# Performance work log

Measured on AMD Instinct MI355X. Metric: run time of the kernel, lower is better.

## Reference

```python
import jax, jax.numpy as jnp
import numpy as np

B, T, D = 16, 4096, 256


def setup_inputs() -> dict:
    key = jax.random.key(0)
    ks = jax.random.split(key, 10)
    s = 1.0 / np.sqrt(D)  # torch nn.Linear default init range
    inp = {
        "x": jax.random.normal(ks[0], (B, T, D), jnp.float32),
        "hidden": jax.random.normal(ks[1], (B, D), jnp.float32),
    }
    names = ["W0", "b0", "W1", "b1", "W2", "b2", "W3", "b3"]
    for i, n in enumerate(names):
        shape = (D, D) if n.startswith("W") else (D,)
        inp[n] = jax.random.uniform(ks[2 + i], shape, jnp.float32, -s, s)
    return inp


def _gln(x, W0, b0, W1, b1, W2, b2, W3, b3):
    # Two gated-linear blocks; the final Linear(hyper[-1], hidden_size) in the
    # original module is never applied by calc_gln (index == len-1 is skipped).
    h = (x @ W0.T + b0) * jax.nn.sigmoid(x @ W1.T + b1)
    return (h @ W2.T + b2) * jax.nn.sigmoid(h @ W3.T + b3)


def reference(x, hidden, W0, b0, W1, b1, W2, b2, W3, b3):
    b = _gln(x, W0, b0, W1, b1, W2, b2, W3, b3)  # [B, T, D]
    bt = jnp.swapaxes(b, 0, 1)  # [T, B, D] for time-major scan
    init = jax.nn.relu(bt[0] + jnp.roll(hidden, 1, -1))

    def step(prev, b_t):
        out = jax.nn.relu(b_t + jnp.roll(prev, 1, -1))
        return out, out

    last, ys = jax.lax.scan(step, init, bt[1:])
    outputs = jnp.concatenate([init[None], ys], axis=0)  # [T, B, D]
    outputs = jnp.swapaxes(outputs, 0, 1)  # [B, T, D]; squeeze(2) is a no-op for D>1
    return outputs, last
```

## Files before the change

kernel.cpp:

```cpp
#include <hip/hip_runtime.h>
#include <hip/hip_bf16.h>
#include <cstdint>
#include <cstddef>

typedef __bf16 bf16x8 __attribute__((ext_vector_type(8)));
typedef float  f32x4  __attribute__((ext_vector_type(4)));

static constexpr int B  = 16;
static constexpr int T  = 4096;
static constexpr int D  = 256;
static constexpr int M  = B * T;
static constexpr int SEGS = 64;
static constexpr int SEGL = T / SEGS;

__global__ void cvt_w(const float* __restrict__ W0, const float* __restrict__ W1,
                      const float* __restrict__ W2, const float* __restrict__ W3,
                      __bf16* __restrict__ wp) {
    int i = blockIdx.x * blockDim.x + threadIdx.x;
    int s    = i >> 14;
    int r    = i & 16383;
    int ks   = r >> 11;
    int fg   = (r >> 6) & 31;
    int lane = r & 63;
    int kg = lane >> 4, rl = lane & 15;
    int w = fg >> 2, f = fg & 3;
    int q = f >> 1, gate = f & 1;
    int rc = w * 32 + 2 * rl + q;
    const float* src = (s == 0) ? (gate ? W1 : W0) : (gate ? W3 : W2);
    const float* p = src + (size_t)rc * 256 + ks * 32 + kg * 8;
    bf16x8 o;
#pragma unroll
    for (int j = 0; j < 8; ++j) o[j] = (__bf16)p[j];
    *reinterpret_cast<bf16x8*>(wp + (size_t)s * 131072 +
                               ((size_t)((ks * 32 + fg) * 64 + lane)) * 8) = o;
}

__launch_bounds__(512, 4)
__global__ void gln_fused(const float* __restrict__ x,
                          const __bf16* __restrict__ wp,
                          const float* __restrict__ b0, const float* __restrict__ b1,
                          const float* __restrict__ b2, const float* __restrict__ b3,
                          float* __restrict__ out,
                          float2* __restrict__ seg_am) {
    extern __shared__ char smem[];
    char* xlds = smem;
    char* hlds = smem + 32768;
    float* ftile = reinterpret_cast<float*>(smem);

    const int tid  = threadIdx.x;
    const int lane = tid & 63;
    const int wid  = tid >> 6;
    const int rl   = lane & 15;
    const int kg   = lane >> 4;
    const int row0 = blockIdx.x * 64;

    const __bf16* wv0 = wp + ((size_t)(wid * 4) * 64 + lane) * 8;
    const __bf16* wv1 = wv0 + 131072;

    bf16x8 bbuf[2][4];
    auto loadB = [&](int p, const __bf16* wvb, int ks) {
#pragma unroll
        for (int f = 0; f < 4; ++f)
            bbuf[p][f] = *reinterpret_cast<const bf16x8*>(wvb + ks * 16384 + f * 512);
    };

    {
        int r  = tid >> 3;
        int c0 = tid & 7;
        const float* xr = x + (size_t)(row0 + r) * 256;
        float4 xa[4][2];
#pragma unroll
        for (int ci = 0; ci < 4; ++ci) {
            const float4* p = reinterpret_cast<const float4*>(xr + (c0 + ci * 8) * 8);
            xa[ci][0] = p[0];
            xa[ci][1] = p[1];
        }
#pragma unroll
        for (int ci = 0; ci < 4; ++ci) {
            int ck = c0 + ci * 8;
            bf16x8 o = { (__bf16)xa[ci][0].x, (__bf16)xa[ci][0].y,
                         (__bf16)xa[ci][0].z, (__bf16)xa[ci][0].w,
                         (__bf16)xa[ci][1].x, (__bf16)xa[ci][1].y,
                         (__bf16)xa[ci][1].z, (__bf16)xa[ci][1].w };
            *reinterpret_cast<bf16x8*>(&xlds[r * 512 + ((ck ^ (r & 7)) * 16)]) = o;
        }
    }
    loadB(0, wv0, 0);
    __syncthreads();

    f32x4 acc[4][4];

    auto run_stage = [&](const char* alds, const __bf16* wvb) {
#pragma unroll
        for (int m = 0; m < 4; ++m)
#pragma unroll
            for (int f = 0; f < 4; ++f) acc[m][f] = (f32x4){0.f, 0.f, 0.f, 0.f};
#pragma unroll
        for (int ks = 0; ks < 8; ++ks) {
            if (ks < 7) loadB((ks + 1) & 1, wvb, ks + 1);
            bf16x8 aR[4];
#pragma unroll
            for (int m = 0; m < 4; ++m) {
                int row = m * 16 + rl;
                int ck  = (ks * 4 + kg) ^ (rl & 7);
                aR[m] = *reinterpret_cast<const bf16x8*>(&alds[row * 512 + ck * 16]);
            }
#pragma unroll
            for (int m = 0; m < 4; ++m)
#pragma unroll
                for (int f = 0; f < 4; ++f)
                    acc[m][f] = __builtin_amdgcn_mfma_f32_16x16x32_bf16(
                        aR[m], bbuf[ks & 1][f], acc[m][f], 0, 0, 0);
        }
    };

    run_stage(xlds, wv0);
    loadB(0, wv1, 0);
    {
        int rc0 = wid * 32 + 2 * rl;
        float2 bb0 = *reinterpret_cast<const float2*>(b0 + rc0);
        float2 bb1 = *reinterpret_cast<const float2*>(b1 + rc0);
        int colb = rc0 * 2;
        int ckb  = colb >> 4;
        int off  = colb & 15;
#pragma unroll
        for (int m = 0; m < 4; ++m)
#pragma unroll
            for (int j = 0; j < 4; ++j) {
                int row = m * 16 + kg * 4 + j;
                float he = (acc[m][0][j] + bb0.x) *
                           (1.0f / (1.0f + __expf(-(acc[m][1][j] + bb1.x))));
                float ho = (acc[m][2][j] + bb0.y) *
                           (1.0f / (1.0f + __expf(-(acc[m][3][j] + bb1.y))));
                unsigned short ue = __builtin_bit_cast(unsigned short, (__bf16)he);
                unsigned short uo = __builtin_bit_cast(unsigned short, (__bf16)ho);
                unsigned int u = ((unsigned int)uo << 16) | (unsigned int)ue;
                *reinterpret_cast<unsigned int*>(
                    &hlds[row * 512 + ((ckb ^ (row & 7)) * 16) + off]) = u;
            }
    }
    __syncthreads();

    run_stage(hlds, wv1);
    __syncthreads();

    float2 ov[16];
    const int rc0 = wid * 32 + 2 * rl;
    {
        float2 bb2 = *reinterpret_cast<const float2*>(b2 + rc0);
        float2 bb3 = *reinterpret_cast<const float2*>(b3 + rc0);
#pragma unroll
        for (int m = 0; m < 4; ++m)
#pragma unroll
            for (int j = 0; j < 4; ++j) {
                int row = m * 16 + kg * 4 + j;
                float he = (acc[m][0][j] + bb2.x) *
                           (1.0f / (1.0f + __expf(-(acc[m][1][j] + bb3.x))));
                float ho = (acc[m][2][j] + bb2.y) *
                           (1.0f / (1.0f + __expf(-(acc[m][3][j] + bb3.y))));
                float2 o; o.x = he; o.y = ho;
                ov[m * 4 + j] = o;
                *reinterpret_cast<float2*>(ftile + row * 256 + rc0) = o;
            }
    }
    __syncthreads();

#pragma unroll
    for (int m = 0; m < 4; ++m)
#pragma unroll
        for (int j = 0; j < 4; ++j) {
            int row = m * 16 + kg * 4 + j;
            *reinterpret_cast<float2*>(out + (size_t)(row0 + row) * 256 + rc0) =
                ov[m * 4 + j];
        }

    if (tid < 256) {
        int c     = tid;
        int batch = row0 >> 12;
        int t0    = row0 & 4095;
        int seg   = t0 >> 6;
        int cc    = (c + t0) & 255;
        float A = 0.f, Mx = -1e30f;
#pragma unroll 8
        for (int i = 0; i < SEGL; ++i) {
            float v = ftile[i * 256 + ((cc + i) & 255)];
            A += v;
            Mx = fmaxf(Mx + v, 0.f);
        }
        float2 o; o.x = A; o.y = Mx;
        seg_am[(size_t)(batch * SEGS + seg) * 256 + c] = o;
    }
}

__global__ void scan_bound(const float2* __restrict__ seg_am,
                           const float* __restrict__ hidden,
                           float* __restrict__ seg_state) {
    int tid   = blockIdx.x * blockDim.x + threadIdx.x;
    int c     = tid & 255;
    int batch = tid >> 8;
    float s = hidden[batch * 256 + ((c + 255) & 255)];
    for (int seg = 0; seg < SEGS; ++seg) {
        seg_state[(size_t)(batch * SEGS + seg) * 256 + c] = s;
        float2 am = seg_am[(size_t)(batch * SEGS + seg) * 256 + c];
        s = fmaxf(s + am.x, am.y);
    }
}

__global__ void scan_apply(float* __restrict__ bio,
                           const float* __restrict__ seg_state,
                           float* __restrict__ last) {
    int tid   = blockIdx.x * blockDim.x + threadIdx.x;
    int c     = tid & 255;
    int rest  = tid >> 8;
    int batch = rest & 15;
    int seg   = rest >> 4;
    float s = seg_state[(size_t)(batch * SEGS + seg) * 256 + c];
    float* base = bio + (size_t)batch * T * D;
    int t0 = seg * SEGL;
#pragma unroll 8
    for (int i = 0; i < SEGL; ++i) {
        int t = t0 + i;
        size_t idx = (size_t)t * 256 + ((c + t) & 255);
        float v = base[idx];
        s = fmaxf(s + v, 0.f);
        base[idx] = s;
    }
    if (seg == SEGS - 1) last[batch * 256 + ((c + 255) & 255)] = s;
}

extern "C" void kernel_launch(void* const* d_in, const int* in_sizes, int n_in,
                              void* d_out, int out_size, void* d_ws, size_t ws_size,
                              hipStream_t stream) {
    const float* x      = (const float*)d_in[0];
    const float* hidden = (const float*)d_in[1];
    const float* W0 = (const float*)d_in[2];
    const float* b0 = (const float*)d_in[3];
    const float* W1 = (const float*)d_in[4];
    const float* b1 = (const float*)d_in[5];
    const float* W2 = (const float*)d_in[6];
    const float* b2 = (const float*)d_in[7];
    const float* W3 = (const float*)d_in[8];
    const float* b3 = (const float*)d_in[9];

    float* out  = (float*)d_out;
    float* last = out + (size_t)M * D;

    char* ws = (char*)d_ws;
    __bf16* wpb       = (__bf16*)ws;
    float2* seg_am    = (float2*)(ws + 524288);
    float*  seg_state = (float*)(ws + 524288 + 2097152);

    static bool attr_done = false;
    if (!attr_done) {
        hipFuncSetAttribute(reinterpret_cast<const void*>(&gln_fused),
                            hipFuncAttributeMaxDynamicSharedMemorySize, 65536);
        attr_done = true;
    }

    cvt_w<<<128, 256, 0, stream>>>(W0, W1, W2, W3, wpb);
    gln_fused<<<M / 64, 512, 65536, stream>>>(x, wpb, b0, b1, b2, b3, out, seg_am);

    scan_bound<<<B * D / 256, 256, 0, stream>>>(seg_am, hidden, seg_state);
    scan_apply<<<(B * D * SEGS) / 256, 256, 0, stream>>>(out, seg_state, last);
}
```

Baseline: 91.52 us.

## Enlarge GLN block tile to 128 rows with 1024 threads and swizzled output tile

The fused gated-linear kernel now processes 128 rows per block with 16 waves instead of 64 rows with 8 waves. Each wave owns 16 output columns (one value and one gate fragment) across all 128 rows, and the packed weight layout is changed to match. Each weight fragment loaded into registers is reused across twice as many rows. The fp32 output tile in LDS gets an XOR swizzle to cut bank conflicts in the segment-scan reads. The costs are 128KB of LDS per block, which limits residency to one block per CU, scalar rather than float2 global stores, and 16-bit LDS stores for the intermediate activations.

```diff
diff --git a/kernel.cpp b/kernel.cpp
--- a/kernel.cpp
+++ b/kernel.cpp
@@ -23,9 +23,8 @@
     int fg   = (r >> 6) & 31;
     int lane = r & 63;
     int kg = lane >> 4, rl = lane & 15;
-    int w = fg >> 2, f = fg & 3;
-    int q = f >> 1, gate = f & 1;
-    int rc = w * 32 + 2 * rl + q;
+    int w = fg >> 1, gate = fg & 1;
+    int rc = w * 16 + rl;
     const float* src = (s == 0) ? (gate ? W1 : W0) : (gate ? W3 : W2);
     const float* p = src + (size_t)rc * 256 + ks * 32 + kg * 8;
     bf16x8 o;
@@ -35,7 +34,7 @@
                                ((size_t)((ks * 32 + fg) * 64 + lane)) * 8) = o;
 }
 
-__launch_bounds__(512, 4)
+__launch_bounds__(1024, 4)
 __global__ void gln_fused(const float* __restrict__ x,
                           const __bf16* __restrict__ wp,
                           const float* __restrict__ b0, const float* __restrict__ b1,
@@ -44,7 +43,7 @@
                           float2* __restrict__ seg_am) {
     extern __shared__ char smem[];
     char* xlds = smem;
-    char* hlds = smem + 32768;
+    char* hlds = smem + 65536;
     float* ftile = reinterpret_cast<float*>(smem);
 
     const int tid  = threadIdx.x;
@@ -52,15 +51,15 @@
     const int wid  = tid >> 6;
     const int rl   = lane & 15;
     const int kg   = lane >> 4;
-    const int row0 = blockIdx.x * 64;
-
-    const __bf16* wv0 = wp + ((size_t)(wid * 4) * 64 + lane) * 8;
+    const int row0 = blockIdx.x * 128;
+
+    const __bf16* wv0 = wp + ((size_t)(wid * 2) * 64 + lane) * 8;
     const __bf16* wv1 = wv0 + 131072;
 
-    bf16x8 bbuf[2][4];
+    bf16x8 bbuf[2][2];
     auto loadB = [&](int p, const __bf16* wvb, int ks) {
 #pragma unroll
-        for (int f = 0; f < 4; ++f)
+        for (int f = 0; f < 2; ++f)
             bbuf[p][f] = *reinterpret_cast<const bf16x8*>(wvb + ks * 16384 + f * 512);
     };
 
@@ -88,55 +87,54 @@
     loadB(0, wv0, 0);
     __syncthreads();
 
-    f32x4 acc[4][4];
+    f32x4 acc[8][2];
 
     auto run_stage = [&](const char* alds, const __bf16* wvb) {
 #pragma unroll
-        for (int m = 0; m < 4; ++m)
-#pragma unroll
-            for (int f = 0; f < 4; ++f) acc[m][f] = (f32x4){0.f, 0.f, 0.f, 0.f};
+        for (int m = 0; m < 8; ++m)
+#pragma unroll
+            for (int f = 0; f < 2; ++f) acc[m][f] = (f32x4){0.f, 0.f, 0.f, 0.f};
 #pragma unroll
         for (int ks = 0; ks < 8; ++ks) {
             if (ks < 7) loadB((ks + 1) & 1, wvb, ks + 1);
-            bf16x8 aR[4];
-#pragma unroll
-            for (int m = 0; m < 4; ++m) {
-                int row = m * 16 + rl;
-                int ck  = (ks * 4 + kg) ^ (rl & 7);
-                aR[m] = *reinterpret_cast<const bf16x8*>(&alds[row * 512 + ck * 16]);
+#pragma unroll
+            for (int mh = 0; mh < 2; ++mh) {
+                bf16x8 aR[4];
+#pragma unroll
+                for (int mi = 0; mi < 4; ++mi) {
+                    int row = (mh * 4 + mi) * 16 + rl;
+                    int ck  = (ks * 4 + kg) ^ (rl & 7);
+                    aR[mi] = *reinterpret_cast<const bf16x8*>(&alds[row * 512 + ck * 16]);
+                }
+#pragma unroll
+                for (int mi = 0; mi < 4; ++mi)
+#pragma unroll
+                    for (int f = 0; f < 2; ++f)
+                        acc[mh * 4 + mi][f] = __builtin_amdgcn_mfma_f32_16x16x32_bf16(
+                            aR[mi], bbuf[ks & 1][f], acc[mh * 4 + mi][f], 0, 0, 0);
             }
-#pragma unroll
-            for (int m = 0; m < 4; ++m)
-#pragma unroll
-                for (int f = 0; f < 4; ++f)
-                    acc[m][f] = __builtin_amdgcn_mfma_f32_16x16x32_bf16(
-                        aR[m], bbuf[ks & 1][f], acc[m][f], 0, 0, 0);
         }
     };
+
+    const int rc = wid * 16 + rl;
 
     run_stage(xlds, wv0);
     loadB(0, wv1, 0);
     {
-        int rc0 = wid * 32 + 2 * rl;
-        float2 bb0 = *reinterpret_cast<const float2*>(b0 + rc0);
-        float2 bb1 = *reinterpret_cast<const float2*>(b1 + rc0);
-        int colb = rc0 * 2;
-        int ckb  = colb >> 4;
-        int off  = colb & 15;
-#pragma unroll
-        for (int m = 0; m < 4; ++m)
+        float bb0 = b0[rc];
+        float bb1 = b1[rc];
+        int cb = rc * 2;
+        int ck = cb >> 4;
+        int off = cb & 15;
+#pragma unroll
+        for (int m = 0; m < 8; ++m)
 #pragma unroll
             for (int j = 0; j < 4; ++j) {
                 int row = m * 16 + kg * 4 + j;
-                float he = (acc[m][0][j] + bb0.x) *
-                           (1.0f / (1.0f + __expf(-(acc[m][1][j] + bb1.x))));
-                float ho = (acc[m][2][j] + bb0.y) *
-                           (1.0f / (1.0f + __expf(-(acc[m][3][j] + bb1.y))));
-                unsigned short ue = __builtin_bit_cast(unsigned short, (__bf16)he);
-                unsigned short uo = __builtin_bit_cast(unsigned short, (__bf16)ho);
-                unsigned int u = ((unsigned int)uo << 16) | (unsigned int)ue;
-                *reinterpret_cast<unsigned int*>(
-                    &hlds[row * 512 + ((ckb ^ (row & 7)) * 16) + off]) = u;
+                float hv = (acc[m][0][j] + bb0) *
+                           (1.0f / (1.0f + __expf(-(acc[m][1][j] + bb1))));
+                *reinterpret_cast<__bf16*>(
+                    &hlds[row * 512 + ((ck ^ (row & 7)) * 16) + off]) = (__bf16)hv;
             }
     }
     __syncthreads();
@@ -144,46 +142,46 @@
     run_stage(hlds, wv1);
     __syncthreads();
 
-    float2 ov[16];
-    const int rc0 = wid * 32 + 2 * rl;
+    float ov[32];
     {
-        float2 bb2 = *reinterpret_cast<const float2*>(b2 + rc0);
-        float2 bb3 = *reinterpret_cast<const float2*>(b3 + rc0);
-#pragma unroll
-        for (int m = 0; m < 4; ++m)
+        float bb2 = b2[rc];
+        float bb3 = b3[rc];
+#pragma unroll
+        for (int m = 0; m < 8; ++m)
 #pragma unroll
             for (int j = 0; j < 4; ++j) {
                 int row = m * 16 + kg * 4 + j;
-                float he = (acc[m][0][j] + bb2.x) *
-                           (1.0f / (1.0f + __expf(-(acc[m][1][j] + bb3.x))));
-                float ho = (acc[m][2][j] + bb2.y) *
-                           (1.0f / (1.0f + __expf(-(acc[m][3][j] + bb3.y))));
-                float2 o; o.x = he; o.y = ho;
-                ov[m * 4 + j] = o;
-                *reinterpret_cast<float2*>(ftile + row * 256 + rc0) = o;
+                float v = (acc[m][0][j] + bb2) *
+                          (1.0f / (1.0f + __expf(-(acc[m][1][j] + bb3))));
+                ov[m * 4 + j] = v;
+                int col = rc ^ ((row & 7) << 2);
+                ftile[row * 256 + col] = v;
             }
     }
     __syncthreads();
 
 #pragma unroll
-    for (int m = 0; m < 4; ++m)
+    for (int m = 0; m < 8; ++m)
 #pragma unroll
         for (int j = 0; j < 4; ++j) {
             int row = m * 16 + kg * 4 + j;
-            *reinterpret_cast<float2*>(out + (size_t)(row0 + row) * 256 + rc0) =
-                ov[m * 4 + j];
-        }
-
-    if (tid < 256) {
-        int c     = tid;
+            out[(size_t)(row0 + row) * 256 + rc] = ov[m * 4 + j];
+        }
+
+    if (tid < 512) {
+        int c     = tid & 255;
+        int sidx  = tid >> 8;
         int batch = row0 >> 12;
-        int t0    = row0 & 4095;
+        int t0    = (row0 & 4095) + sidx * 64;
         int seg   = t0 >> 6;
         int cc    = (c + t0) & 255;
+        int rbase = sidx * 64;
         float A = 0.f, Mx = -1e30f;
 #pragma unroll 8
         for (int i = 0; i < SEGL; ++i) {
-            float v = ftile[i * 256 + ((cc + i) & 255)];
+            int row = rbase + i;
+            int col = ((cc + i) & 255) ^ ((row & 7) << 2);
+            float v = ftile[row * 256 + col];
             A += v;
             Mx = fmaxf(Mx + v, 0.f);
         }
@@ -253,12 +251,12 @@
     static bool attr_done = false;
     if (!attr_done) {
         hipFuncSetAttribute(reinterpret_cast<const void*>(&gln_fused),
-                            hipFuncAttributeMaxDynamicSharedMemorySize, 65536);
+                            hipFuncAttributeMaxDynamicSharedMemorySize, 131072);
         attr_done = true;
     }
 
     cvt_w<<<128, 256, 0, stream>>>(W0, W1, W2, W3, wpb);
-    gln_fused<<<M / 64, 512, 65536, stream>>>(x, wpb, b0, b1, b2, b3, out, seg_am);
+    gln_fused<<<M / 128, 1024, 131072, stream>>>(x, wpb, b0, b1, b2, b3, out, seg_am);
 
     scan_bound<<<B * D / 256, 256, 0, stream>>>(seg_am, hidden, seg_state);
     scan_apply<<<(B * D * SEGS) / 256, 256, 0, stream>>>(out, seg_state, last);
```

Result: slower. 102.0 us (+11.5%).
